# Kernel tuning notes

Measured on AMD Instinct MI355X. Metric: run time of the kernel, lower is better.

The kernel has to match this reference:

```python
import jax, jax.numpy as jnp
import numpy as np

B, S, D = 2, 2048, 2048
H, DN, DR, DV = 16, 128, 64, 128   # heads, qk_nope, qk_rope, v_head
Q_LORA, KV_LORA = 1536, 512
DQ = DN + DR                        # qk_head_dim = 192
EPS = 1e-6


def setup_inputs() -> dict:
    key = jax.random.key(0)
    ks = jax.random.split(key, 8)
    s = 0.02  # weight init scale
    hidden_states = jax.random.normal(ks[0], (B, S, D), jnp.float32)
    # RoPE tables (non-interleaved HF style: cat(freqs, freqs)) per position
    inv_freq = 1.0 / (10000.0 ** (np.arange(0, DR, 2, dtype=np.float32) / DR))
    freqs = np.arange(S, dtype=np.float32)[:, None] * inv_freq[None, :]  # [S, DR/2]
    emb = np.concatenate([freqs, freqs], axis=-1)                        # [S, DR]
    cos = jnp.broadcast_to(jnp.asarray(np.cos(emb)), (B, S, DR))
    sin = jnp.broadcast_to(jnp.asarray(np.sin(emb)), (B, S, DR))
    return {
        'hidden_states': hidden_states,
        'cos': cos, 'sin': sin,
        'Wqa': jax.random.normal(ks[1], (D, Q_LORA), jnp.float32) * s,
        'qa_ln_w': jnp.ones((Q_LORA,), jnp.float32),
        'Wqb': jax.random.normal(ks[2], (Q_LORA, H * DQ), jnp.float32) * s,
        'Wkva': jax.random.normal(ks[3], (D, KV_LORA + DR), jnp.float32) * s,
        'kva_ln_w': jnp.ones((KV_LORA,), jnp.float32),
        'Wkvb': jax.random.normal(ks[4], (KV_LORA, H * (DN + DV)), jnp.float32) * s,
        'Wo': jax.random.normal(ks[5], (H * DV, D), jnp.float32) * s,
    }


def _rmsnorm(x, w):
    xf = x.astype(jnp.float32)
    var = jnp.mean(xf * xf, axis=-1, keepdims=True)
    return w * (xf * jax.lax.rsqrt(var + EPS)).astype(x.dtype)


def _rotate_half(x):
    h = x.shape[-1] // 2
    return jnp.concatenate([-x[..., h:], x[..., :h]], axis=-1)


def reference(hidden_states, cos, sin, Wqa, qa_ln_w, Wqb, Wkva, kva_ln_w, Wkvb, Wo):
    b, s, _ = hidden_states.shape
    scaling = DQ ** -0.5

    # Q path: down-proj -> RMSNorm -> up-proj -> [b, H, s, DQ]
    q = _rmsnorm(hidden_states @ Wqa, qa_ln_w) @ Wqb
    q = q.reshape(b, s, H, DQ).transpose(0, 2, 1, 3)
    q_pass, q_rot = q[..., :DN], q[..., DN:]

    # KV path: joint down-proj -> split latent / shared rope key
    ckv = hidden_states @ Wkva                       # [b, s, KV_LORA + DR]
    k_lat, k_rot = ckv[..., :KV_LORA], ckv[..., KV_LORA:]
    kv = _rmsnorm(k_lat, kva_ln_w) @ Wkvb            # [b, s, H*(DN+DV)]
    kv = kv.reshape(b, s, H, DN + DV).transpose(0, 2, 1, 3)
    k_pass, v = kv[..., :DN], kv[..., DN:]

    # decoupled RoPE on q_rot and the single shared k_rot head
    k_rot = k_rot[:, None, :, :]                     # [b, 1, s, DR]
    c, si = cos[:, None], sin[:, None]               # unsqueeze_dim=1
    q_rot = q_rot * c + _rotate_half(q_rot) * si
    k_rot = k_rot * c + _rotate_half(k_rot) * si
    k_rot = jnp.broadcast_to(k_rot, (b, H, s, DR))

    Q = jnp.concatenate([q_pass, q_rot], axis=-1)    # [b, H, s, DQ]
    K = jnp.concatenate([k_pass, k_rot], axis=-1)

    scores = jnp.einsum('bhqd,bhkd->bhqk', Q, K) * scaling
    neg = jnp.finfo(jnp.float32).min
    causal = jnp.where(jnp.tril(jnp.ones((s, s), bool)), 0.0, neg)
    scores = scores + causal
    w = jax.nn.softmax(scores.astype(jnp.float32), axis=-1).astype(Q.dtype)

    out = jnp.einsum('bhqk,bhkd->bhqd', w, v)
    out = out.transpose(0, 2, 1, 3).reshape(b, s, H * DV)
    return out @ Wo
```

## Files before the change

### kernel.cpp

```cpp
#include <hip/hip_runtime.h>
#include <math.h>

#define BB 2
#define SS 2048
#define DD 2048
#define HH 16
#define DN 128
#define DR 64
#define DV 128
#define QL 1536
#define KVL 512
#define DQ 192
#define CKVS 640
#define KVD 256
#define NCAT 2176
#define NCATP 2304
#define EPSF 1e-6f

typedef short bfrag __attribute__((ext_vector_type(8)));
typedef float facc  __attribute__((ext_vector_type(4)));

__device__ __forceinline__ ushort f2bf(float f) {
    union { float f; unsigned u; } v; v.f = f;
    unsigned r = v.u + 0x7fffu + ((v.u >> 16) & 1u);
    return (ushort)(r >> 16);
}
__device__ __forceinline__ float bf2f(ushort u) {
    union { unsigned u; float f; } v; v.u = ((unsigned)u) << 16;
    return v.f;
}
__device__ __forceinline__ float fexp2(float x) {
    float r; asm("v_exp_f32 %0, %1" : "=v"(r) : "v"(x)); return r;
}
__device__ __forceinline__ float wave_red_sum(float v) {
    #pragma unroll
    for (int o = 32; o > 0; o >>= 1) v += __shfl_down(v, o);
    return v;
}
__device__ __forceinline__ void gl2lds16(const ushort* g, ushort* l) {
    __builtin_amdgcn_global_load_lds(
        (const __attribute__((address_space(1))) void*)g,
        (__attribute__((address_space(3))) void*)l, 16, 0, 0);
}
__device__ __forceinline__ void storeC(float* c, float v)  { *c = v; }
__device__ __forceinline__ void storeC(ushort* c, float v) { *c = f2bf(v); }

__global__ __launch_bounds__(256) void castf2bf(const float* __restrict__ x,
                                                ushort* __restrict__ y) {
    const int i = blockIdx.x * 256 + threadIdx.x;
    const float4 v = ((const float4*)x)[i];
    ushort4 o;
    o.x = f2bf(v.x); o.y = f2bf(v.y); o.z = f2bf(v.z); o.w = f2bf(v.w);
    ((ushort4*)y)[i] = o;
}

struct WtBatch {
    const float* src[5];
    ushort* dst[5];
    int K[5];
    int N[5];
    int nx[5];
    int base[6];
};
__global__ __launch_bounds__(256) void wtrans_b(WtBatch d) {
    __shared__ float tile[32][33];
    int bid = blockIdx.x;
    int seg = 0;
    while (bid >= d.base[seg + 1]) ++seg;
    const int l = bid - d.base[seg];
    const int nx = d.nx[seg];
    const int bx = l % nx, by = l / nx;
    const float* W = d.src[seg];
    ushort* Wt = d.dst[seg];
    const int K = d.K[seg], N = d.N[seg];
    const int k0 = by * 32, n0 = bx * 32;
    const int t = threadIdx.x;
    const int tx = t & 31, ty = t >> 5;
    #pragma unroll
    for (int r = 0; r < 4; ++r) {
        const int n = n0 + tx;
        tile[ty + r * 8][tx] =
            (n < N) ? W[(size_t)(k0 + ty + r * 8) * N + n] : 0.f;
    }
    __syncthreads();
    #pragma unroll
    for (int r = 0; r < 4; ++r) {
        const int n = n0 + ty + r * 8;
        Wt[(size_t)n * K + k0 + tx] = f2bf(tile[tx][ty + r * 8]);
    }
}


__device__ __forceinline__ void stage_half(const ushort* __restrict__ G,
                                           int ldg, int grow0, int kcol0,
                                           ushort* Lr, int wave, int lane) {
    const int r0   = lane >> 3;
    const int slot = (lane & 7) ^ r0;
    const ushort* s0 = G + (size_t)(grow0 + wave * 16 + r0) * ldg + kcol0 + slot * 8;
    gl2lds16(s0,                    Lr + wave * 1024);
    gl2lds16(s0 + (size_t)8 * ldg,  Lr + wave * 1024 + 512);
}

#define PH_PRE  do { __builtin_amdgcn_sched_barrier(0);                      \
                     __builtin_amdgcn_s_barrier();                           \
                     asm volatile("s_waitcnt lgkmcnt(0)" ::: "memory");      \
                     __builtin_amdgcn_sched_barrier(0);                      \
                     __builtin_amdgcn_s_setprio(1); } while (0)
#define PH_POST do { __builtin_amdgcn_s_setprio(0);                          \
                     __builtin_amdgcn_sched_barrier(0);                      \
                     __builtin_amdgcn_s_barrier(); } while (0)

#define MFMA16(RB)                                                           \
    _Pragma("unroll")                                                        \
    for (int i = 0; i < 4; ++i)                                              \
        _Pragma("unroll")                                                    \
        for (int j = 0; j < 4; ++j)                                          \
            acc[(RB) + i][j] = __builtin_amdgcn_mfma_f32_16x16x32_bf16(      \
                a[i], b[j], acc[(RB) + i][j], 0, 0, 0);

#define GEMM256_CORE(A_, Bt_, K_, NBX_)                                       \
    __shared__ ushort L[65536];                           \
    const int t    = threadIdx.x;                                             \
    const int lane = t & 63;                                                  \
    const int wave = t >> 6;                                                  \
    const int wm   = wave >> 2;                                               \
    const int wn   = wave & 3;                                                \
    const int quad = lane >> 4;                                               \
    const int lrow = lane & 15;                                               \
    int wg = (int)blockIdx.x;                                                 \
    { const int cpx = (int)gridDim.x >> 3; wg = (wg & 7) * cpx + (wg >> 3); } \
    const int bx = wg % (NBX_), by = wg / (NBX_);                             \
    const int m0 = by * 256, n0 = bx * 256;                                   \
    const int s0x8  = (quad ^ (lrow & 7)) * 8;       \
    const int s1x8  = s0x8 ^ 32;                   \
    const int abase = lrow * 64;                                              \
    const int bbase = (wn & 1) * 4096 + lrow * 64;                            \
    facc acc[8][4];                                                           \
    _Pragma("unroll")                                                         \
    for (int i = 0; i < 8; ++i)                                               \
        _Pragma("unroll")                                                     \
        for (int j = 0; j < 4; ++j) acc[i][j] = (facc)(0.f);                  \
    const int nk = (K_) >> 6;                                                 \
                  \
    stage_half((A_),  (K_), m0,        0, L,         wave, lane);             \
    stage_half((A_),  (K_), m0 + 128,  0, L + 8192,  wave, lane);             \
    stage_half((Bt_), (K_), n0,        0, L + 16384, wave, lane);             \
    stage_half((Bt_), (K_), n0 + 128,  0, L + 24576, wave, lane);             \
    stage_half((Bt_), (K_), n0,       64, L + 49152, wave, lane);             \
    stage_half((Bt_), (K_), n0 + 128, 64, L + 57344, wave, lane);             \
    asm volatile("s_waitcnt vmcnt(4)" ::: "memory");                          \
    __builtin_amdgcn_s_barrier();                                             \
    for (int kt = 0; kt < nk; ++kt) {                                         \
        const int p = kt & 1;                                                 \
        ushort* LA = L + p * 32768 + wm * 8192;                               \
        ushort* LB = L + p * 32768 + 16384 + (wn >> 1) * 8192;                \
        ushort* Lq = L + (p ^ 1) * 32768;                                     \
        const int kn = (kt + 1) * 64;                                         \
        bfrag a[4], b[4];                                                     \
                                           \
        _Pragma("unroll")                                                     \
        for (int i = 0; i < 4; ++i)                                           \
            a[i] = *(const bfrag*)(LA + i * 1024 + abase + s0x8);             \
        _Pragma("unroll")                                                     \
        for (int j = 0; j < 4; ++j)                                           \
            b[j] = *(const bfrag*)(LB + bbase + j * 1024 + s0x8);             \
        if (kt + 1 < nk) stage_half((A_), (K_), m0, kn, Lq, wave, lane);      \
        PH_PRE;                                                               \
        MFMA16(0)                                                             \
        PH_POST;                                                              \
                                \
        _Pragma("unroll")                                                     \
        for (int i = 0; i < 4; ++i)                                           \
            a[i] = *(const bfrag*)(LA + (4 + i) * 1024 + abase + s0x8);       \
        if (kt + 1 < nk)                                                      \
            stage_half((A_), (K_), m0 + 128, kn, Lq + 8192, wave, lane);      \
        PH_PRE;                                                               \
        MFMA16(4)                                                             \
        PH_POST;                                                              \
                                           \
        _Pragma("unroll")                                                     \
        for (int i = 0; i < 4; ++i)                                           \
            a[i] = *(const bfrag*)(LA + i * 1024 + abase + s1x8);             \
        _Pragma("unroll")                                                     \
        for (int j = 0; j < 4; ++j)                                           \
            b[j] = *(const bfrag*)(LB + bbase + j * 1024 + s1x8);             \
        PH_PRE;                                                               \
        MFMA16(0)                                                             \
        PH_POST;                                                              \
             \
        _Pragma("unroll")                                                     \
        for (int i = 0; i < 4; ++i)                                           \
            a[i] = *(const bfrag*)(LA + (4 + i) * 1024 + abase + s1x8);       \
        if (kt + 2 < nk) {                                                    \
            stage_half((Bt_), (K_), n0,       kn + 64,                        \
                       L + p * 32768 + 16384, wave, lane);                    \
            stage_half((Bt_), (K_), n0 + 128, kn + 64,                        \
                       L + p * 32768 + 24576, wave, lane);                    \
            asm volatile("s_waitcnt vmcnt(4)" ::: "memory");                  \
        } else {                                                              \
            asm volatile("s_waitcnt vmcnt(0)" ::: "memory");                  \
        }                                                                     \
        PH_PRE;                                                               \
        MFMA16(4)                                                             \
        PH_POST;                                                              \
    }

template <typename OUT, int K, int NBX, int NOUT>
__global__ __launch_bounds__(512, 2) void gemm256(const ushort* __restrict__ A,
                                                  const ushort* __restrict__ Bt,
                                                  OUT* __restrict__ C) {
    GEMM256_CORE(A, Bt, K, NBX)
    #pragma unroll
    for (int m = 0; m < 8; ++m) {
        const int row = m0 + wm * 128 + m * 16 + quad * 4;
        #pragma unroll
        for (int nf = 0; nf < 4; ++nf) {
            const int col = n0 + wn * 64 + nf * 16 + lrow;
            #pragma unroll
            for (int r = 0; r < 4; ++r)
                storeC(&C[(size_t)(row + r) * NOUT + col], acc[m][nf][r]);
        }
    }
}

template <int K, int NBX, int NOUT>
__global__ __launch_bounds__(512, 2) void gemmW(const ushort* __restrict__ A,
                                                const ushort* __restrict__ Bt,
                                                float* __restrict__ C) {
    __shared__ ushort L[57344];
    const int t    = threadIdx.x;
    const int lane = t & 63;
    const int wave = t >> 6;
    const int wm   = wave >> 1;
    const int wn   = wave & 1;
    const int quad = lane >> 4;
    const int lrow = lane & 15;
    int wg = (int)blockIdx.x;
    { const int cpx = (int)gridDim.x >> 3; wg = (wg & 7) * cpx + (wg >> 3); }
    const int bx = wg % NBX, by = wg / NBX;
    const int m0 = by * 256, n0 = bx * 128;
    const int s0x8 = (quad ^ (lrow & 7)) * 8;
    const int s1x8 = s0x8 ^ 32;
    facc acc[4][4];
    #pragma unroll
    for (int i = 0; i < 4; ++i)
        #pragma unroll
        for (int j = 0; j < 4; ++j) acc[i][j] = (facc)(0.f);
    const int nk = K >> 6;
    stage_half(A,  K, m0,        0, L,          wave, lane);
    stage_half(A,  K, m0 + 128,  0, L + 8192,   wave, lane);
    stage_half(Bt, K, n0,        0, L + 32768,  wave, lane);
    stage_half(Bt, K, n0,       64, L + 40960,  wave, lane);
    asm volatile("s_waitcnt vmcnt(0)" ::: "memory");
    __builtin_amdgcn_s_barrier();
    int bp = 0, bp2 = 2;
    for (int kt = 0; kt < nk; ++kt) {
        const int p = kt & 1;
        ushort* LA = L + p * 16384 + (wm >> 1) * 8192
                       + ((wm & 1) * 64 + lrow) * 64;
        ushort* LB = L + 32768 + bp * 8192 + (wn * 64 + lrow) * 64;
        const int kn = (kt + 1) * 64;
        bfrag a[4], b[4];
        #pragma unroll
        for (int i = 0; i < 4; ++i) a[i] = *(const bfrag*)(LA + i * 1024 + s0x8);
        #pragma unroll
        for (int j = 0; j < 4; ++j) b[j] = *(const bfrag*)(LB + j * 1024 + s0x8);
        if (kt + 1 < nk) {
            stage_half(A, K, m0,       kn, L + (p ^ 1) * 16384,        wave, lane);
            stage_half(A, K, m0 + 128, kn, L + (p ^ 1) * 16384 + 8192, wave, lane);
        }
        if (kt + 2 < nk)
            stage_half(Bt, K, n0, kn + 64, L + 32768 + bp2 * 8192, wave, lane);
        PH_PRE;
        MFMA16(0)
        PH_POST;
        #pragma unroll
        for (int i = 0; i < 4; ++i) a[i] = *(const bfrag*)(LA + i * 1024 + s1x8);
        #pragma unroll
        for (int j = 0; j < 4; ++j) b[j] = *(const bfrag*)(LB + j * 1024 + s1x8);
        if (kt + 2 < nk) { asm volatile("s_waitcnt vmcnt(2)" ::: "memory"); }
        else             { asm volatile("s_waitcnt vmcnt(0)" ::: "memory"); }
        PH_PRE;
        MFMA16(0)
        PH_POST;
        bp  = (bp  == 2) ? 0 : bp  + 1;
        bp2 = (bp2 == 2) ? 0 : bp2 + 1;
    }
    #pragma unroll
    for (int m = 0; m < 4; ++m) {
        const int row = m0 + wm * 64 + m * 16 + quad * 4;
        #pragma unroll
        for (int nf = 0; nf < 4; ++nf) {
            const int col = n0 + wn * 64 + nf * 16 + lrow;
            #pragma unroll
            for (int r = 0; r < 4; ++r)
                C[(size_t)(row + r) * NOUT + col] = acc[m][nf][r];
        }
    }
}

__global__ __launch_bounds__(512, 2) void gemmA256(const ushort* __restrict__ A,
                                                   const ushort* __restrict__ Bt,
                                                   ushort* __restrict__ qa,
                                                   ushort* __restrict__ ckv) {
    GEMM256_CORE(A, Bt, DD, 9)
    #pragma unroll
    for (int m = 0; m < 8; ++m) {
        const int row = m0 + wm * 128 + m * 16 + quad * 4;
        #pragma unroll
        for (int nf = 0; nf < 4; ++nf) {
            const int col = n0 + wn * 64 + nf * 16 + lrow;
            #pragma unroll
            for (int r = 0; r < 4; ++r) {
                if (col < QL)
                    qa[(size_t)(row + r) * QL + col] = f2bf(acc[m][nf][r]);
                else if (col < NCAT)
                    ckv[(size_t)(row + r) * CKVS + col - QL] = f2bf(acc[m][nf][r]);
            }
        }
    }
}

__global__ __launch_bounds__(512, 2) void gemmQ256(const ushort* __restrict__ A,
                                                   const ushort* __restrict__ Bt,
                                                   ushort* __restrict__ Qbuf) {
    GEMM256_CORE(A, Bt, QL, 12)
    const float scaling = 0.10411754831f;
    #pragma unroll
    for (int m = 0; m < 8; ++m) {
        const int row = m0 + wm * 128 + m * 16 + quad * 4;
        #pragma unroll
        for (int nf = 0; nf < 4; ++nf) {
            const int col = n0 + wn * 64 + nf * 16 + lrow;
            const int h = col / DQ, d = col - h * DQ;
            #pragma unroll
            for (int r = 0; r < 4; ++r) {
                const int tok = row + r;
                const int b = tok >> 11, s = tok & (SS - 1);
                Qbuf[((size_t)(b * HH + h) * SS + s) * DQ + d] =
                    f2bf(acc[m][nf][r] * scaling);
            }
        }
    }
}

__global__ __launch_bounds__(256) void rmsnorm_bf_ip(ushort* __restrict__ x,
                                                     const float* __restrict__ w,
                                                     int n) {
    ushort* xr = x + (size_t)blockIdx.x * n;
    const int t = threadIdx.x;
    float ss = 0.f;
    for (int i = t; i < n; i += 256) { float v = bf2f(xr[i]); ss += v * v; }
    ss = wave_red_sum(ss);
    __shared__ float red[4];
    const int lane = t & 63, wid = t >> 6;
    if (lane == 0) red[wid] = ss;
    __syncthreads();
    const float tot = red[0] + red[1] + red[2] + red[3];
    const float scale = rsqrtf(tot / (float)n + EPSF);
    for (int i = t; i < n; i += 256) xr[i] = f2bf(w[i] * bf2f(xr[i]) * scale);
}

__global__ __launch_bounds__(256) void rmsnorm_kv(const ushort* __restrict__ x,
                                                  const float* __restrict__ w,
                                                  ushort* __restrict__ y,
                                                  ushort* __restrict__ krb,
                                                  const float* __restrict__ cosb,
                                                  const float* __restrict__ sinb) {
    const int row = blockIdx.x;
    const ushort* xr = x + (size_t)row * CKVS;
    ushort* yr = y + (size_t)row * KVL;
    const int t = threadIdx.x;
    if (t < 64) {
        const int p = t;
        const ushort* kin = xr + KVL;
        const float c  = cosb[(size_t)row * DR + p];
        const float sn = sinb[(size_t)row * DR + p];
        const float self = bf2f(kin[p]);
        const float partner = bf2f(kin[p < 32 ? p + 32 : p - 32]);
        const float v = (p < 32) ? (self * c - partner * sn)
                                 : (self * c + partner * sn);
        krb[(size_t)row * DR + p] = f2bf(v);
    }
    float ss = 0.f;
    for (int i = t; i < KVL; i += 256) { float v = bf2f(xr[i]); ss += v * v; }
    ss = wave_red_sum(ss);
    __shared__ float red[4];
    const int lane = t & 63, wid = t >> 6;
    if (lane == 0) red[wid] = ss;
    __syncthreads();
    const float tot = red[0] + red[1] + red[2] + red[3];
    const float scale = rsqrtf(tot / (float)KVL + EPSF);
    for (int i = t; i < KVL; i += 256) yr[i] = f2bf(w[i] * bf2f(xr[i]) * scale);
}

__global__ __launch_bounds__(256) void qrope(ushort* __restrict__ Qbuf,
                                             const float* __restrict__ cosb,
                                             const float* __restrict__ sinb) {
    const int tok = blockIdx.x;
    const int b = tok >> 11, s = tok & (SS - 1);
    const int t = threadIdx.x;
    const int p = t & 31, hh = t >> 5;
    const float c0 = cosb[(size_t)tok * DR + p];
    const float s0 = sinb[(size_t)tok * DR + p];
    const float c1 = cosb[(size_t)tok * DR + p + 32];
    const float s1 = sinb[(size_t)tok * DR + p + 32];
    #pragma unroll
    for (int it = 0; it < 2; ++it) {
        const int h = hh + it * 8;
        ushort* base = Qbuf + ((size_t)(b * HH + h) * SS + s) * DQ + DN;
        const float x0 = bf2f(base[p]), x1 = bf2f(base[p + 32]);
        base[p]      = f2bf(x0 * c0 - x1 * s0);
        base[p + 32] = f2bf(x1 * c1 + x0 * s1);
    }
}

__global__ __launch_bounds__(256) void vprep(const ushort* __restrict__ kv_bf,
                                             ushort* __restrict__ Vtb) {
    __shared__ ushort tile[32][33];
    const int kp0 = blockIdx.x * 32, dv0 = blockIdx.y * 32, bh = blockIdx.z;
    const int b = bh / HH, h = bh - b * HH;
    const int t = threadIdx.x, tx = t & 31, ty = t >> 5;
    #pragma unroll
    for (int r = 0; r < 4; ++r)
        tile[ty + r * 8][tx] =
            kv_bf[(size_t)(b * SS + kp0 + ty + r * 8) * (HH * KVD) + h * KVD + DN + dv0 + tx];
    __syncthreads();
    #pragma unroll
    for (int r = 0; r < 4; ++r)
        Vtb[((size_t)bh * DV + dv0 + ty + r * 8) * SS + kp0 + tx] = tile[tx][ty + r * 8];
}

__global__ __launch_bounds__(256, 2) void fattn_mfma(
    const ushort* __restrict__ Qb,
    const ushort* __restrict__ kvb,
    const ushort* __restrict__ krb,
    const ushort* __restrict__ Vt,
    ushort* __restrict__ o)
{
    const int h  = blockIdx.y;
    const int b  = blockIdx.z;
    const int qt = b ? (15 - (int)blockIdx.x) : (int)blockIdx.x;
    const int bh = b * HH + h;
    const int q0 = qt * 128;
    const int t    = threadIdx.x;
    const int lane = t & 63;
    const int wave = t >> 6;
    const int quad = lane >> 4;
    const int n    = lane & 15;
    const int wstrip = wave * 16;

    __shared__ ushort Ksu[6 * 64 * 32];
    __shared__ ushort Vtu[2 * 128 * 32];
    __shared__ ushort Psu[2 * 128 * 40];

    const ushort* vbase = Vt + (size_t)bh * DV * SS;

    bfrag aQ[2][6];
    #pragma unroll
    for (int sp = 0; sp < 2; ++sp) {
        const ushort* qrow = Qb + ((size_t)bh * SS + q0 + sp * 64 + wstrip + n) * DQ;
        #pragma unroll
        for (int kb = 0; kb < 6; ++kb)
            aQ[sp][kb] = *(const bfrag*)(qrow + kb * 32 + quad * 8);
    }

    facc oacc[2][8];
    float lp[2][4];
    #pragma unroll
    for (int sp = 0; sp < 2; ++sp) {
        #pragma unroll
        for (int jd = 0; jd < 8; ++jd) oacc[sp][jd] = (facc)(0.f);
        #pragma unroll
        for (int r = 0; r < 4; ++r) lp[sp][r] = 0.f;
    }

    #pragma unroll
    for (int i = 0; i < 6; ++i) {
        const int g = wave + 4 * i;
        const int kb = g >> 2;
        const int rem = (g & 3) * 64 + lane;
        const int row = rem >> 2, sub = rem & 3;
        const int tok = b * SS + row;
        const ushort* src = (kb < 4)
            ? kvb + (size_t)tok * (HH * KVD) + h * KVD + kb * 32 + sub * 8
            : krb + (size_t)tok * DR + (kb - 4) * 32 + sub * 8;
        gl2lds16(src, Ksu + g * 512);
    }
    #pragma unroll
    for (int i = 0; i < 4; ++i) {
        const int g = wave + 4 * i;
        const int kb2 = g >> 3;
        const int rem = (g & 7) * 64 + lane;
        const int dv = rem >> 2, sub = rem & 3;
        gl2lds16(vbase + (size_t)dv * SS + kb2 * 32 + sub * 8, Vtu + g * 512);
    }
    __syncthreads();

    const int nkt = 2 * qt + 2;
    for (int kt = 0; kt < nkt; ++kt) {
        const int k0 = kt * 64;
        const int k1 = k0 + 64;
        const bool more = (kt + 1 < nkt);

        bfrag kreg[6], vreg[4];
        if (more) {
            #pragma unroll
            for (int i = 0; i < 6; ++i) {
                const int g = wave + 4 * i;
                const int kb = g >> 2;
                const int rem = (g & 3) * 64 + lane;
                const int row = rem >> 2, sub = rem & 3;
                const int tok = b * SS + k1 + row;
                const ushort* src = (kb < 4)
                    ? kvb + (size_t)tok * (HH * KVD) + h * KVD + kb * 32 + sub * 8
                    : krb + (size_t)tok * DR + (kb - 4) * 32 + sub * 8;
                kreg[i] = *(const bfrag*)src;
            }
            #pragma unroll
            for (int i = 0; i < 4; ++i) {
                const int g = wave + 4 * i;
                const int kb2 = g >> 3;
                const int rem = (g & 7) * 64 + lane;
                const int dv = rem >> 2, sub = rem & 3;
                vreg[i] = *(const bfrag*)(vbase + (size_t)dv * SS + k1 + kb2 * 32 + sub * 8);
            }
        }
        __builtin_amdgcn_sched_barrier(0);

        facc s[2][4];
        #pragma unroll
        for (int sp = 0; sp < 2; ++sp)
            #pragma unroll
            for (int j = 0; j < 4; ++j) s[sp][j] = (facc)(0.f);
        #pragma unroll
        for (int kb = 0; kb < 6; ++kb) {
            #pragma unroll
            for (int j = 0; j < 4; ++j) {
                const bfrag bk =
                    *(const bfrag*)&Ksu[kb * 2048 + (j * 16 + n) * 32 + quad * 8];
                s[0][j] = __builtin_amdgcn_mfma_f32_16x16x32_bf16(aQ[0][kb], bk, s[0][j], 0, 0, 0);
                s[1][j] = __builtin_amdgcn_mfma_f32_16x16x32_bf16(aQ[1][kb], bk, s[1][j], 0, 0, 0);
            }
        }

        const bool fullt = (k1 <= q0);
        if (fullt) {
            #pragma unroll
            for (int sp = 0; sp < 2; ++sp) {
                #pragma unroll
                for (int j = 0; j < 4; ++j) {
                    #pragma unroll
                    for (int r = 0; r < 4; ++r) {
                        const float p = fexp2(s[sp][j][r]);
                        lp[sp][r] += p;
                        Psu[(j >> 1) * 5120 + (sp * 64 + wstrip + quad * 4 + r) * 40
                            + (j & 1) * 16 + n] = f2bf(p);
                    }
                }
            }
        } else {
            #pragma unroll
            for (int sp = 0; sp < 2; ++sp) {
                const int rowg0 = q0 + sp * 64 + wstrip + quad * 4;
                #pragma unroll
                for (int j = 0; j < 4; ++j) {
                    const int kpos = k0 + j * 16 + n;
                    #pragma unroll
                    for (int r = 0; r < 4; ++r) {
                        const float p = (kpos <= rowg0 + r) ? fexp2(s[sp][j][r]) : 0.f;
                        lp[sp][r] += p;
                        Psu[(j >> 1) * 5120 + (sp * 64 + wstrip + quad * 4 + r) * 40
                            + (j & 1) * 16 + n] = f2bf(p);
                    }
                }
            }
        }

        #pragma unroll
        for (int kb2 = 0; kb2 < 2; ++kb2) {
            const bfrag aP0 = *(const bfrag*)&Psu[kb2 * 5120 + (wstrip + n) * 40 + quad * 8];
            const bfrag aP1 = *(const bfrag*)&Psu[kb2 * 5120 + (64 + wstrip + n) * 40 + quad * 8];
            #pragma unroll
            for (int jd = 0; jd < 8; ++jd) {
                const bfrag bV = *(const bfrag*)&Vtu[kb2 * 4096 + (jd * 16 + n) * 32 + quad * 8];
                oacc[0][jd] = __builtin_amdgcn_mfma_f32_16x16x32_bf16(aP0, bV, oacc[0][jd], 0, 0, 0);
                oacc[1][jd] = __builtin_amdgcn_mfma_f32_16x16x32_bf16(aP1, bV, oacc[1][jd], 0, 0, 0);
            }
        }

        __syncthreads();
        if (more) {
            #pragma unroll
            for (int i = 0; i < 6; ++i)
                *(bfrag*)(Ksu + (wave + 4 * i) * 512 + lane * 8) = kreg[i];
            #pragma unroll
            for (int i = 0; i < 4; ++i)
                *(bfrag*)(Vtu + (wave + 4 * i) * 512 + lane * 8) = vreg[i];
        }
        __syncthreads();
    }

    #pragma unroll
    for (int sp = 0; sp < 2; ++sp) {
        #pragma unroll
        for (int r = 0; r < 4; ++r) {
            float v = lp[sp][r];
            #pragma unroll
            for (int msk = 1; msk < 16; msk <<= 1) v += __shfl_xor(v, msk);
            const float inv = 1.f / v;
            ushort* op = o + (size_t)(b * SS + q0 + sp * 64 + wstrip + quad * 4 + r)
                             * (HH * DV) + h * DV;
            #pragma unroll
            for (int jd = 0; jd < 8; ++jd)
                op[jd * 16 + n] = f2bf(oacc[sp][jd][r] * inv);
        }
    }
}

extern "C" void kernel_launch(void* const* d_in, const int* in_sizes, int n_in,
                              void* d_out, int out_size, void* d_ws, size_t ws_size,
                              hipStream_t stream) {
    const float* hs    = (const float*)d_in[0];
    const float* cosb  = (const float*)d_in[1];
    const float* sinb  = (const float*)d_in[2];
    const float* Wqa   = (const float*)d_in[3];
    const float* qa_w  = (const float*)d_in[4];
    const float* Wqb   = (const float*)d_in[5];
    const float* Wkva  = (const float*)d_in[6];
    const float* kva_w = (const float*)d_in[7];
    const float* Wkvb  = (const float*)d_in[8];
    const float* Wo    = (const float*)d_in[9];
    float* out = (float*)d_out;

    const int T = BB * SS;

    char* w = (char*)d_ws;
    auto alloc = [&](size_t bytes) {
        void* r = (void*)w;
        w += (bytes + 255) & ~(size_t)255;
        return r;
    };
    ushort* hs_bf  = (ushort*)alloc((size_t)T * DD * 2);
    ushort* Wcat   = (ushort*)alloc((size_t)NCATP * DD * 2);
    ushort* Wqbt   = (ushort*)alloc((size_t)(HH * DQ) * QL * 2);
    ushort* Wkvbt  = (ushort*)alloc((size_t)(HH * KVD) * KVL * 2);
    ushort* Wot    = (ushort*)alloc((size_t)DD * DD * 2);
    ushort* qa_bf  = (ushort*)alloc((size_t)T * QL * 2);
    ushort* Qbuf   = (ushort*)alloc((size_t)T * HH * DQ * 2);
    ushort* ckv_bf = (ushort*)alloc((size_t)T * CKVS * 2);
    ushort* kvn_bf = (ushort*)alloc((size_t)T * KVL * 2);
    ushort* kv_bf  = (ushort*)alloc((size_t)T * HH * KVD * 2);
    ushort* krb    = (ushort*)alloc((size_t)T * DR * 2);
    ushort* Vtb    = Wcat;
    ushort* ao_bf  = hs_bf;

    castf2bf<<<(T * DD / 4) / 256, 256, 0, stream>>>(hs, hs_bf);
    WtBatch wb;
    wb.src[0] = Wqa;  wb.dst[0] = Wcat;                      wb.K[0] = DD;  wb.N[0] = QL;       wb.nx[0] = 48;
    wb.src[1] = Wkva; wb.dst[1] = Wcat + (size_t)QL * DD;    wb.K[1] = DD;  wb.N[1] = KVL + DR; wb.nx[1] = 20;
    wb.src[2] = Wqb;  wb.dst[2] = Wqbt;                      wb.K[2] = QL;  wb.N[2] = HH * DQ;  wb.nx[2] = 96;
    wb.src[3] = Wkvb; wb.dst[3] = Wkvbt;                     wb.K[3] = KVL; wb.N[3] = HH * KVD; wb.nx[3] = 128;
    wb.src[4] = Wo;   wb.dst[4] = Wot;                       wb.K[4] = DD;  wb.N[4] = DD;       wb.nx[4] = 64;
    wb.base[0] = 0;
    wb.base[1] = wb.base[0] + wb.nx[0] * (DD / 32);
    wb.base[2] = wb.base[1] + wb.nx[1] * (DD / 32);
    wb.base[3] = wb.base[2] + wb.nx[2] * (QL / 32);
    wb.base[4] = wb.base[3] + wb.nx[3] * (KVL / 32);
    wb.base[5] = wb.base[4] + wb.nx[4] * (DD / 32);
    wtrans_b<<<wb.base[5], 256, 0, stream>>>(wb);

    gemmA256<<<dim3(9 * 16), 512, 0, stream>>>(hs_bf, Wcat, qa_bf, ckv_bf);
    rmsnorm_bf_ip<<<T, 256, 0, stream>>>(qa_bf, qa_w, QL);
    gemmQ256<<<dim3(12 * 16), 512, 0, stream>>>(qa_bf, Wqbt, Qbuf);
    qrope<<<T, 256, 0, stream>>>(Qbuf, cosb, sinb);
    rmsnorm_kv<<<T, 256, 0, stream>>>(ckv_bf, kva_w, kvn_bf, krb, cosb, sinb);
    gemm256<ushort, KVL, 16, HH * KVD><<<dim3(16 * 16), 512, 0, stream>>>(kvn_bf, Wkvbt, kv_bf);
    vprep<<<dim3(SS / 32, DV / 32, BB * HH), 256, 0, stream>>>(kv_bf, Vtb);
    fattn_mfma<<<dim3(16, HH, BB), 256, 0, stream>>>(Qbuf, kv_bf, krb, Vtb, ao_bf);
    gemmW<DD, 16, DD><<<dim3(256), 512, 0, stream>>>(ao_bf, Wot, out);
}
```

Before: 430.1 us.

## Merge independent launches into combined kernels and drop branch in attention prefetch

Horizontally fuses independent kernels: the two RMSNorms become one launch, the Q and KV up-projection GEMMs become one 448-block launch, and the Q RoPE plus V transpose become one launch. This cuts kernel launches from seven to four and lets the smaller KV GEMM fill the GPU alongside the Q GEMM. In the attention loop, the K/V prefetch now runs unconditionally, loading a dummy tile on the last iteration, so the `more` branch disappears at the cost of one redundant load and LDS store per block.

New measurement: 423.3 us. No clear change (-1.6%).

```diff
diff --git a/kernel.cpp b/kernel.cpp
--- a/kernel.cpp
+++ b/kernel.cpp
@@ -42,8 +42,6 @@
         (const __attribute__((address_space(1))) void*)g,
         (__attribute__((address_space(3))) void*)l, 16, 0, 0);
 }
-__device__ __forceinline__ void storeC(float* c, float v)  { *c = v; }
-__device__ __forceinline__ void storeC(ushort* c, float v) { *c = f2bf(v); }
 
 __global__ __launch_bounds__(256) void castf2bf(const float* __restrict__ x,
                                                 ushort* __restrict__ y) {
@@ -118,8 +116,7 @@
             acc[(RB) + i][j] = __builtin_amdgcn_mfma_f32_16x16x32_bf16(      \
                 a[i], b[j], acc[(RB) + i][j], 0, 0, 0);
 
-#define GEMM256_CORE(A_, Bt_, K_, NBX_)                                       \
-    __shared__ ushort L[65536];                           \
+#define GEMM256_CORE(A_, Bt_, K_, NBX_, LID_)                                 \
     const int t    = threadIdx.x;                                             \
     const int lane = t & 63;                                                  \
     const int wave = t >> 6;                                                  \
@@ -127,9 +124,7 @@
     const int wn   = wave & 3;                                                \
     const int quad = lane >> 4;                                               \
     const int lrow = lane & 15;                                               \
-    int wg = (int)blockIdx.x;                                                 \
-    { const int cpx = (int)gridDim.x >> 3; wg = (wg & 7) * cpx + (wg >> 3); } \
-    const int bx = wg % (NBX_), by = wg / (NBX_);                             \
+    const int bx = (LID_) % (NBX_), by = (LID_) / (NBX_);                     \
     const int m0 = by * 256, n0 = bx * 256;                                   \
     const int s0x8  = (quad ^ (lrow & 7)) * 8;       \
     const int s1x8  = s0x8 ^ 32;                   \
@@ -205,24 +200,6 @@
         PH_POST;                                                              \
     }
 
-template <typename OUT, int K, int NBX, int NOUT>
-__global__ __launch_bounds__(512, 2) void gemm256(const ushort* __restrict__ A,
-                                                  const ushort* __restrict__ Bt,
-                                                  OUT* __restrict__ C) {
-    GEMM256_CORE(A, Bt, K, NBX)
-    #pragma unroll
-    for (int m = 0; m < 8; ++m) {
-        const int row = m0 + wm * 128 + m * 16 + quad * 4;
-        #pragma unroll
-        for (int nf = 0; nf < 4; ++nf) {
-            const int col = n0 + wn * 64 + nf * 16 + lrow;
-            #pragma unroll
-            for (int r = 0; r < 4; ++r)
-                storeC(&C[(size_t)(row + r) * NOUT + col], acc[m][nf][r]);
-        }
-    }
-}
-
 template <int K, int NBX, int NOUT>
 __global__ __launch_bounds__(512, 2) void gemmW(const ushort* __restrict__ A,
                                                 const ushort* __restrict__ Bt,
@@ -303,7 +280,9 @@
                                                    const ushort* __restrict__ Bt,
                                                    ushort* __restrict__ qa,
                                                    ushort* __restrict__ ckv) {
-    GEMM256_CORE(A, Bt, DD, 9)
+    __shared__ ushort L[65536];
+    const int lid = ((int)blockIdx.x & 7) * 18 + ((int)blockIdx.x >> 3);
+    GEMM256_CORE(A, Bt, DD, 9, lid)
     #pragma unroll
     for (int m = 0; m < 8; ++m) {
         const int row = m0 + wm * 128 + m * 16 + quad * 4;
@@ -321,114 +300,139 @@
     }
 }
 
-__global__ __launch_bounds__(512, 2) void gemmQ256(const ushort* __restrict__ A,
-                                                   const ushort* __restrict__ Bt,
-                                                   ushort* __restrict__ Qbuf) {
-    GEMM256_CORE(A, Bt, QL, 12)
-    const float scaling = 0.10411754831f;
-    #pragma unroll
-    for (int m = 0; m < 8; ++m) {
-        const int row = m0 + wm * 128 + m * 16 + quad * 4;
-        #pragma unroll
-        for (int nf = 0; nf < 4; ++nf) {
-            const int col = n0 + wn * 64 + nf * 16 + lrow;
-            const int h = col / DQ, d = col - h * DQ;
-            #pragma unroll
-            for (int r = 0; r < 4; ++r) {
-                const int tok = row + r;
-                const int b = tok >> 11, s = tok & (SS - 1);
-                Qbuf[((size_t)(b * HH + h) * SS + s) * DQ + d] =
-                    f2bf(acc[m][nf][r] * scaling);
+__global__ __launch_bounds__(512, 2) void gemmQKV(
+    const ushort* __restrict__ qa,  const ushort* __restrict__ Wqbt,
+    ushort* __restrict__ Qbuf,
+    const ushort* __restrict__ kvn, const ushort* __restrict__ Wkvbt,
+    ushort* __restrict__ kvb) {
+    __shared__ ushort L[65536];
+    const int bid = (int)blockIdx.x;
+    if (bid < 192) {
+        const int lid = (bid & 7) * 24 + (bid >> 3);
+        GEMM256_CORE(qa, Wqbt, QL, 12, lid)
+        const float scaling = 0.10411754831f;
+        #pragma unroll
+        for (int m = 0; m < 8; ++m) {
+            const int row = m0 + wm * 128 + m * 16 + quad * 4;
+            #pragma unroll
+            for (int nf = 0; nf < 4; ++nf) {
+                const int col = n0 + wn * 64 + nf * 16 + lrow;
+                const int h = col / DQ, d = col - h * DQ;
+                #pragma unroll
+                for (int r = 0; r < 4; ++r) {
+                    const int tok = row + r;
+                    const int b = tok >> 11, s = tok & (SS - 1);
+                    Qbuf[((size_t)(b * HH + h) * SS + s) * DQ + d] =
+                        f2bf(acc[m][nf][r] * scaling);
+                }
             }
         }
-    }
-}
-
-__global__ __launch_bounds__(256) void rmsnorm_bf_ip(ushort* __restrict__ x,
-                                                     const float* __restrict__ w,
-                                                     int n) {
-    ushort* xr = x + (size_t)blockIdx.x * n;
+    } else {
+        const int b2 = bid - 192;
+        const int lid = (b2 & 7) * 32 + (b2 >> 3);
+        GEMM256_CORE(kvn, Wkvbt, KVL, 16, lid)
+        #pragma unroll
+        for (int m = 0; m < 8; ++m) {
+            const int row = m0 + wm * 128 + m * 16 + quad * 4;
+            #pragma unroll
+            for (int nf = 0; nf < 4; ++nf) {
+                const int col = n0 + wn * 64 + nf * 16 + lrow;
+                #pragma unroll
+                for (int r = 0; r < 4; ++r)
+                    kvb[(size_t)(row + r) * (HH * KVD) + col] = f2bf(acc[m][nf][r]);
+            }
+        }
+    }
+}
+
+__global__ __launch_bounds__(256) void rmsnorm2(ushort* __restrict__ qa,
+                                                const float* __restrict__ qaw,
+                                                const ushort* __restrict__ ckv,
+                                                const float* __restrict__ kvw,
+                                                ushort* __restrict__ kvn,
+                                                ushort* __restrict__ krb,
+                                                const float* __restrict__ cosb,
+                                                const float* __restrict__ sinb) {
+    __shared__ float red[4];
     const int t = threadIdx.x;
-    float ss = 0.f;
-    for (int i = t; i < n; i += 256) { float v = bf2f(xr[i]); ss += v * v; }
-    ss = wave_red_sum(ss);
-    __shared__ float red[4];
     const int lane = t & 63, wid = t >> 6;
-    if (lane == 0) red[wid] = ss;
-    __syncthreads();
-    const float tot = red[0] + red[1] + red[2] + red[3];
-    const float scale = rsqrtf(tot / (float)n + EPSF);
-    for (int i = t; i < n; i += 256) xr[i] = f2bf(w[i] * bf2f(xr[i]) * scale);
-}
-
-__global__ __launch_bounds__(256) void rmsnorm_kv(const ushort* __restrict__ x,
-                                                  const float* __restrict__ w,
-                                                  ushort* __restrict__ y,
-                                                  ushort* __restrict__ krb,
-                                                  const float* __restrict__ cosb,
-                                                  const float* __restrict__ sinb) {
-    const int row = blockIdx.x;
-    const ushort* xr = x + (size_t)row * CKVS;
-    ushort* yr = y + (size_t)row * KVL;
+    const int bid = (int)blockIdx.x;
+    if (bid < BB * SS) {
+        ushort* xr = qa + (size_t)bid * QL;
+        float ss = 0.f;
+        for (int i = t; i < QL; i += 256) { float v = bf2f(xr[i]); ss += v * v; }
+        ss = wave_red_sum(ss);
+        if (lane == 0) red[wid] = ss;
+        __syncthreads();
+        const float tot = red[0] + red[1] + red[2] + red[3];
+        const float sc = rsqrtf(tot / (float)QL + EPSF);
+        for (int i = t; i < QL; i += 256) xr[i] = f2bf(qaw[i] * bf2f(xr[i]) * sc);
+    } else {
+        const int row = bid - BB * SS;
+        const ushort* xr = ckv + (size_t)row * CKVS;
+        ushort* yr = kvn + (size_t)row * KVL;
+        if (t < 64) {
+            const int p = t;
+            const ushort* kin = xr + KVL;
+            const float c  = cosb[(size_t)row * DR + p];
+            const float sn = sinb[(size_t)row * DR + p];
+            const float self = bf2f(kin[p]);
+            const float partner = bf2f(kin[p < 32 ? p + 32 : p - 32]);
+            const float v = (p < 32) ? (self * c - partner * sn)
+                                     : (self * c + partner * sn);
+            krb[(size_t)row * DR + p] = f2bf(v);
+        }
+        float ss = 0.f;
+        for (int i = t; i < KVL; i += 256) { float v = bf2f(xr[i]); ss += v * v; }
+        ss = wave_red_sum(ss);
+        if (lane == 0) red[wid] = ss;
+        __syncthreads();
+        const float tot = red[0] + red[1] + red[2] + red[3];
+        const float sc = rsqrtf(tot / (float)KVL + EPSF);
+        for (int i = t; i < KVL; i += 256) yr[i] = f2bf(kvw[i] * bf2f(xr[i]) * sc);
+    }
+}
+
+__global__ __launch_bounds__(256) void ropevprep(ushort* __restrict__ Qbuf,
+                                                 const float* __restrict__ cosb,
+                                                 const float* __restrict__ sinb,
+                                                 const ushort* __restrict__ kvb,
+                                                 ushort* __restrict__ Vtb) {
+    __shared__ ushort tile[32][33];
+    const int bid = (int)blockIdx.x;
     const int t = threadIdx.x;
-    if (t < 64) {
-        const int p = t;
-        const ushort* kin = xr + KVL;
-        const float c  = cosb[(size_t)row * DR + p];
-        const float sn = sinb[(size_t)row * DR + p];
-        const float self = bf2f(kin[p]);
-        const float partner = bf2f(kin[p < 32 ? p + 32 : p - 32]);
-        const float v = (p < 32) ? (self * c - partner * sn)
-                                 : (self * c + partner * sn);
-        krb[(size_t)row * DR + p] = f2bf(v);
-    }
-    float ss = 0.f;
-    for (int i = t; i < KVL; i += 256) { float v = bf2f(xr[i]); ss += v * v; }
-    ss = wave_red_sum(ss);
-    __shared__ float red[4];
-    const int lane = t & 63, wid = t >> 6;
-    if (lane == 0) red[wid] = ss;
-    __syncthreads();
-    const float tot = red[0] + red[1] + red[2] + red[3];
-    const float scale = rsqrtf(tot / (float)KVL + EPSF);
-    for (int i = t; i < KVL; i += 256) yr[i] = f2bf(w[i] * bf2f(xr[i]) * scale);
-}
-
-__global__ __launch_bounds__(256) void qrope(ushort* __restrict__ Qbuf,
-                                             const float* __restrict__ cosb,
-                                             const float* __restrict__ sinb) {
-    const int tok = blockIdx.x;
-    const int b = tok >> 11, s = tok & (SS - 1);
-    const int t = threadIdx.x;
-    const int p = t & 31, hh = t >> 5;
-    const float c0 = cosb[(size_t)tok * DR + p];
-    const float s0 = sinb[(size_t)tok * DR + p];
-    const float c1 = cosb[(size_t)tok * DR + p + 32];
-    const float s1 = sinb[(size_t)tok * DR + p + 32];
-    #pragma unroll
-    for (int it = 0; it < 2; ++it) {
-        const int h = hh + it * 8;
-        ushort* base = Qbuf + ((size_t)(b * HH + h) * SS + s) * DQ + DN;
-        const float x0 = bf2f(base[p]), x1 = bf2f(base[p + 32]);
-        base[p]      = f2bf(x0 * c0 - x1 * s0);
-        base[p + 32] = f2bf(x1 * c1 + x0 * s1);
-    }
-}
-
-__global__ __launch_bounds__(256) void vprep(const ushort* __restrict__ kv_bf,
-                                             ushort* __restrict__ Vtb) {
-    __shared__ ushort tile[32][33];
-    const int kp0 = blockIdx.x * 32, dv0 = blockIdx.y * 32, bh = blockIdx.z;
-    const int b = bh / HH, h = bh - b * HH;
-    const int t = threadIdx.x, tx = t & 31, ty = t >> 5;
-    #pragma unroll
-    for (int r = 0; r < 4; ++r)
-        tile[ty + r * 8][tx] =
-            kv_bf[(size_t)(b * SS + kp0 + ty + r * 8) * (HH * KVD) + h * KVD + DN + dv0 + tx];
-    __syncthreads();
-    #pragma unroll
-    for (int r = 0; r < 4; ++r)
-        Vtb[((size_t)bh * DV + dv0 + ty + r * 8) * SS + kp0 + tx] = tile[tx][ty + r * 8];
+    if (bid < BB * SS) {
+        const int tok = bid;
+        const int b = tok >> 11, s = tok & (SS - 1);
+        const int p = t & 31, hh = t >> 5;
+        const float c0 = cosb[(size_t)tok * DR + p];
+        const float s0 = sinb[(size_t)tok * DR + p];
+        const float c1 = cosb[(size_t)tok * DR + p + 32];
+        const float s1 = sinb[(size_t)tok * DR + p + 32];
+        #pragma unroll
+        for (int it = 0; it < 2; ++it) {
+            const int h = hh + it * 8;
+            ushort* base = Qbuf + ((size_t)(b * HH + h) * SS + s) * DQ + DN;
+            const float x0 = bf2f(base[p]), x1 = bf2f(base[p + 32]);
+            base[p]      = f2bf(x0 * c0 - x1 * s0);
+            base[p + 32] = f2bf(x1 * c1 + x0 * s1);
+        }
+    } else {
+        const int v = bid - BB * SS;
+        const int kp0 = (v & 63) * 32;
+        const int dv0 = ((v >> 6) & 3) * 32;
+        const int bh  = v >> 8;
+        const int b = bh / HH, h = bh - b * HH;
+        const int tx = t & 31, ty = t >> 5;
+        #pragma unroll
+        for (int r = 0; r < 4; ++r)
+            tile[ty + r * 8][tx] =
+                kvb[(size_t)(b * SS + kp0 + ty + r * 8) * (HH * KVD) + h * KVD + DN + dv0 + tx];
+        __syncthreads();
+        #pragma unroll
+        for (int r = 0; r < 4; ++r)
+            Vtb[((size_t)bh * DV + dv0 + ty + r * 8) * SS + kp0 + tx] = tile[tx][ty + r * 8];
+    }
 }
 
 __global__ __launch_bounds__(256, 2) void fattn_mfma(
@@ -500,31 +504,29 @@
     const int nkt = 2 * qt + 2;
     for (int kt = 0; kt < nkt; ++kt) {
         const int k0 = kt * 64;
-        const int k1 = k0 + 64;
         const bool more = (kt + 1 < nkt);
+        const int kk = more ? (k0 + 64) : (SS - 64);
 
         bfrag kreg[6], vreg[4];
-        if (more) {
-            #pragma unroll
-            for (int i = 0; i < 6; ++i) {
-                const int g = wave + 4 * i;
-                const int kb = g >> 2;
-                const int rem = (g & 3) * 64 + lane;
-                const int row = rem >> 2, sub = rem & 3;
-                const int tok = b * SS + k1 + row;
-                const ushort* src = (kb < 4)
-                    ? kvb + (size_t)tok * (HH * KVD) + h * KVD + kb * 32 + sub * 8
-                    : krb + (size_t)tok * DR + (kb - 4) * 32 + sub * 8;
-                kreg[i] = *(const bfrag*)src;
-            }
-            #pragma unroll
-            for (int i = 0; i < 4; ++i) {
-                const int g = wave + 4 * i;
-                const int kb2 = g >> 3;
-                const int rem = (g & 7) * 64 + lane;
-                const int dv = rem >> 2, sub = rem & 3;
-                vreg[i] = *(const bfrag*)(vbase + (size_t)dv * SS + k1 + kb2 * 32 + sub * 8);
-            }
+        #pragma unroll
+        for (int i = 0; i < 6; ++i) {
+            const int g = wave + 4 * i;
+            const int kb = g >> 2;
+            const int rem = (g & 3) * 64 + lane;
+            const int row = rem >> 2, sub = rem & 3;
+            const int tok = b * SS + kk + row;
+            const ushort* src = (kb < 4)
+                ? kvb + (size_t)tok * (HH * KVD) + h * KVD + kb * 32 + sub * 8
+                : krb + (size_t)tok * DR + (kb - 4) * 32 + sub * 8;
+            kreg[i] = *(const bfrag*)src;
+        }
+        #pragma unroll
+        for (int i = 0; i < 4; ++i) {
+            const int g = wave + 4 * i;
+            const int kb2 = g >> 3;
+            const int rem = (g & 7) * 64 + lane;
+            const int dv = rem >> 2, sub = rem & 3;
+            vreg[i] = *(const bfrag*)(vbase + (size_t)dv * SS + kk + kb2 * 32 + sub * 8);
         }
         __builtin_amdgcn_sched_barrier(0);
 
@@ -544,7 +546,7 @@
             }
         }
 
-        const bool fullt = (k1 <= q0);
+        const bool fullt = (k0 + 64 <= q0);
         if (fullt) {
             #pragma unroll
             for (int sp = 0; sp < 2; ++sp) {
@@ -590,14 +592,12 @@
         }
 
         __syncthreads();
-        if (more) {
-            #pragma unroll
-            for (int i = 0; i < 6; ++i)
-                *(bfrag*)(Ksu + (wave + 4 * i) * 512 + lane * 8) = kreg[i];
-            #pragma unroll
-            for (int i = 0; i < 4; ++i)
-                *(bfrag*)(Vtu + (wave + 4 * i) * 512 + lane * 8) = vreg[i];
-        }
+        #pragma unroll
+        for (int i = 0; i < 6; ++i)
+            *(bfrag*)(Ksu + (wave + 4 * i) * 512 + lane * 8) = kreg[i];
+        #pragma unroll
+        for (int i = 0; i < 4; ++i)
+            *(bfrag*)(Vtu + (wave + 4 * i) * 512 + lane * 8) = vreg[i];
         __syncthreads();
     }
 
@@ -670,13 +670,12 @@
     wb.base[5] = wb.base[4] + wb.nx[4] * (DD / 32);
     wtrans_b<<<wb.base[5], 256, 0, stream>>>(wb);
 
-    gemmA256<<<dim3(9 * 16), 512, 0, stream>>>(hs_bf, Wcat, qa_bf, ckv_bf);
-    rmsnorm_bf_ip<<<T, 256, 0, stream>>>(qa_bf, qa_w, QL);
-    gemmQ256<<<dim3(12 * 16), 512, 0, stream>>>(qa_bf, Wqbt, Qbuf);
-    qrope<<<T, 256, 0, stream>>>(Qbuf, cosb, sinb);
-    rmsnorm_kv<<<T, 256, 0, stream>>>(ckv_bf, kva_w, kvn_bf, krb, cosb, sinb);
-    gemm256<ushort, KVL, 16, HH * KVD><<<dim3(16 * 16), 512, 0, stream>>>(kvn_bf, Wkvbt, kv_bf);
-    vprep<<<dim3(SS / 32, DV / 32, BB * HH), 256, 0, stream>>>(kv_bf, Vtb);
+    gemmA256<<<dim3(144), 512, 0, stream>>>(hs_bf, Wcat, qa_bf, ckv_bf);
+    rmsnorm2<<<2 * T, 256, 0, stream>>>(qa_bf, qa_w, ckv_bf, kva_w, kvn_bf,
+                                        krb, cosb, sinb);
+    gemmQKV<<<dim3(448), 512, 0, stream>>>(qa_bf, Wqbt, Qbuf,
+                                           kvn_bf, Wkvbt, kv_bf);
+    ropevprep<<<T + 8192, 256, 0, stream>>>(Qbuf, cosb, sinb, kv_bf, Vtb);
     fattn_mfma<<<dim3(16, HH, BB), 256, 0, stream>>>(Qbuf, kv_bf, krb, Vtb, ao_bf);
     gemmW<DD, 16, DD><<<dim3(256), 512, 0, stream>>>(ao_bf, Wot, out);
 }
```
